# Optimization experiments

Measured on AMD Instinct MI355X. Metric: run time of the kernel, lower is better.

## Reference

```python
import jax, jax.numpy as jnp
import numpy as np

BUCKET_SIZE = 64  # must divide seq_len


def setup_inputs() -> dict:
    key = jax.random.key(0)
    k1, k2, k3, k4 = jax.random.split(key, 4)
    B, S, D = 4, 4096, 1024
    query = jax.random.normal(k1, (B, S, D), dtype=jnp.float32)
    key_t = jax.random.normal(k2, (B, S, D), dtype=jnp.float32)
    value = jax.random.normal(k3, (B, S, D), dtype=jnp.float32)
    # random hashing hyperplanes: [B, D, bucket_size // 2]
    R = jax.random.normal(k4, (B, D, BUCKET_SIZE // 2), dtype=jnp.float32)
    return {"query": query, "key": key_t, "value": value, "R": R}


def reference(query, key, value, R):
    B, S, D = query.shape
    # random projection: [B, S, bucket_size // 2]
    xR = jnp.einsum("bsd,bdr->bsr", query, R)
    # mirror trick -> [B, S, bucket_size]
    concat_xR = jnp.concatenate([xR, -xR], axis=-1)
    buckets = jnp.argmax(concat_xR, axis=-1)          # [B, S] int
    sticker = jnp.argsort(buckets, axis=-1)            # token permutation into buckets
    undo_sort = jnp.argsort(sticker, axis=-1)          # computed in original (unused)
    # batched gather (tf.gather batch_dims=1, axis=1)
    sorted_query = jnp.take_along_axis(query, sticker[..., None], axis=1)
    sorted_value = jnp.take_along_axis(value, sticker[..., None], axis=1)
    # tf.split(x, bucket_size, 1) then stack(axis=1) == reshape to chunks
    chunked_query = sorted_query.reshape(B, BUCKET_SIZE, S // BUCKET_SIZE, D)
    chunked_value = sorted_value.reshape(B, BUCKET_SIZE, S // BUCKET_SIZE, D)
    del undo_sort, chunked_query, chunked_value  # dead code in original; module returns sticker
    return sticker
```

## Files before the change

kernel.cpp:

```cpp
#include <hip/hip_runtime.h>


#define B_DIM 4
#define S_LEN 4096
#define D_DIM 1024
#define NRR 32
#define NBK 64
#define TMK 64
#define NCHUNK (S_LEN / TMK)
#define QB 4096

typedef const __attribute__((address_space(1))) void* gas_t;
typedef __attribute__((address_space(3))) void* las_t;

#define FMA4(A, S, B)                                                        \
    (A).x = fmaf((S), (B).x, (A).x); (A).y = fmaf((S), (B).y, (A).y);        \
    (A).z = fmaf((S), (B).z, (A).z); (A).w = fmaf((S), (B).w, (A).w);

__global__ void __launch_bounds__(256) __attribute__((amdgpu_waves_per_eu(1, 1)))
k1_buckets(const float* __restrict__ Q, const float* __restrict__ R,
           int* __restrict__ buckets, int* __restrict__ hist)
{
    __shared__ float4 smem4[QB + 2048];
    __shared__ int cnt[NBK];

    const int t = threadIdx.x;
    const int b = blockIdx.x >> 6;
    const int chunk = blockIdx.x & 63;

    const int w = t >> 6;
    const int lane = t & 63;
    const int tok_t = lane >> 5;
    const int r_t = (lane >> 3) & 3;
    const int kl = lane & 7;

    const float4* Qw4 = (const float4*)(Q + ((size_t)b * S_LEN + chunk * TMK + w * 16) * D_DIM);
    const float4* Rg4 = (const float4*)(R + (size_t)b * D_DIM * NRR);

#define STAGE_R(H)                                                            \
    {                                                                         \
        _Pragma("unroll")                                                     \
        for (int i = 0; i < 16; ++i) {                                        \
            const int rel = w * 1024 + i * 64 + lane;                         \
            const int kh = rel >> 3, v = rel & 7;                             \
            __builtin_amdgcn_global_load_lds(                                 \
                (gas_t)(Rg4 + ((size_t)(H) * 512 + kh) * 8 + (v ^ ((kh >> 3) & 7))), \
                (las_t)&smem4[w * 1024 + i * 64], 16, 0, 0);                  \
        }                                                                     \
    }

#define ISSUE_Q(H, TILE, DST)                                                 \
    {                                                                         \
        _Pragma("unroll")                                                     \
        for (int i = 0; i < 4; ++i) {                                         \
            const int f = i * 64 + lane;                                      \
            const int td = f >> 4, sd = f & 15;                               \
            __builtin_amdgcn_global_load_lds(                                 \
                (gas_t)(Qw4 + (size_t)td * 256 + (H) * 128 + (TILE) * 16      \
                        + (sd ^ (td >> 3))),                                  \
                (las_t)&smem4[QB + w * 512 + (DST) * 256 + i * 64], 16, 0, 0);\
        }                                                                     \
    }

#define COMPUTE(TILE, BUF)                                                    \
    {                                                                         \
        const float4* qb = smem4 + QB + w * 512 + (BUF) * 256;                \
        const float4* rb = smem4;                                             \
        _Pragma("unroll")                                                     \
        for (int kap = 0; kap < 2; ++kap) {                                   \
            float4 qv[8];                                                     \
            _Pragma("unroll")                                                 \
            for (int j = 0; j < 8; ++j)                                       \
                qv[j] = qb[(tok_t * 8 + j) * 16 + (((kl << 1) + kap) ^ tok_t)];\
            _Pragma("unroll")                                                 \
            for (int c = 0; c < 4; ++c) {                                     \
                const int krow = (TILE) * 64 + kl * 8 + kap * 4 + c;          \
                const float4 rv0 = rb[krow * 8 + ((r_t * 2 + 0) ^ kl)];       \
                const float4 rv1 = rb[krow * 8 + ((r_t * 2 + 1) ^ kl)];       \
                _Pragma("unroll")                                             \
                for (int j = 0; j < 8; ++j) {                                 \
                    const float s = c == 0 ? qv[j].x : c == 1 ? qv[j].y       \
                                  : c == 2 ? qv[j].z : qv[j].w;               \
                    FMA4(acc[j][0], s, rv0);                                  \
                    FMA4(acc[j][1], s, rv1);                                  \
                }                                                             \
            }                                                                 \
        }                                                                     \
    }

    float4 acc[8][2];
#pragma unroll
    for (int j = 0; j < 8; ++j) {
        acc[j][0] = make_float4(0.f, 0.f, 0.f, 0.f);
        acc[j][1] = make_float4(0.f, 0.f, 0.f, 0.f);
    }
    if (t < NBK) cnt[t] = 0;

    for (int h = 0; h < 2; ++h) {
        STAGE_R(h)
        ISSUE_Q(h, 0, 0)
        asm volatile("s_waitcnt vmcnt(0)" ::: "memory");
        __syncthreads();

        for (int tau = 0; tau < 8; ++tau) {
            if (tau < 7) {
                ISSUE_Q(h, tau + 1, (tau + 1) & 1)
                asm volatile("s_waitcnt vmcnt(4)" ::: "memory");
            } else {
                asm volatile("s_waitcnt vmcnt(0)" ::: "memory");
            }
            COMPUTE(tau, tau & 1)
        }
        __syncthreads();
    }
#undef STAGE_R
#undef ISSUE_Q
#undef COMPUTE

#pragma unroll
    for (int j = 0; j < 8; ++j)
#pragma unroll
        for (int p = 0; p < 2; ++p)
#pragma unroll
            for (int off = 1; off < 8; off <<= 1) {
                acc[j][p].x += __shfl_xor(acc[j][p].x, off, 64);
                acc[j][p].y += __shfl_xor(acc[j][p].y, off, 64);
                acc[j][p].z += __shfl_xor(acc[j][p].z, off, 64);
                acc[j][p].w += __shfl_xor(acc[j][p].w, off, 64);
            }

    int bkarr[8];
#pragma unroll
    for (int j = 0; j < 8; ++j) {
        const int rbase = r_t * 8;
        float m1 = acc[j][0].x; int i1 = rbase;
        float m2 = m1;          int i2 = rbase;
#pragma unroll
        for (int p = 0; p < 2; ++p)
#pragma unroll
            for (int c = 0; c < 4; ++c) {
                if (p == 0 && c == 0) continue;
                const float v = p == 0
                    ? (c == 1 ? acc[j][0].y : c == 2 ? acc[j][0].z : acc[j][0].w)
                    : (c == 0 ? acc[j][1].x : c == 1 ? acc[j][1].y
                              : c == 2 ? acc[j][1].z : acc[j][1].w);
                const int r = rbase + p * 4 + c;
                if (v > m1) { m1 = v; i1 = r; }
                if (v < m2) { m2 = v; i2 = r; }
            }
#pragma unroll
        for (int off = 8; off <= 16; off <<= 1) {
            const float om1 = __shfl_xor(m1, off, 64);
            const int   oi1 = __shfl_xor(i1, off, 64);
            const float om2 = __shfl_xor(m2, off, 64);
            const int   oi2 = __shfl_xor(i2, off, 64);
            if (om1 > m1 || (om1 == m1 && oi1 < i1)) { m1 = om1; i1 = oi1; }
            if (om2 < m2 || (om2 == m2 && oi2 < i2)) { m2 = om2; i2 = oi2; }
        }
        bkarr[j] = (m1 >= -m2) ? i1 : (NRR + i2);
    }

    if ((lane & 31) == 0) {
#pragma unroll
        for (int j = 0; j < 8; ++j) {
            const int gtok = chunk * TMK + w * 16 + tok_t * 8 + j;
            buckets[(size_t)b * S_LEN + gtok] = bkarr[j];
            atomicAdd(&cnt[bkarr[j]], 1);
        }
    }
    __syncthreads();
    if (t < NBK) hist[((size_t)b * NCHUNK + chunk) * NBK + t] = cnt[t];
}

__global__ __launch_bounds__(256) void k2_scan(
    const int* __restrict__ hist, int* __restrict__ chunkOffset)
{
    const int t = threadIdx.x;
    const int b = t >> 6;
    const int bk = t & 63;
    const int lane = t & 63;

    int total = 0;
    for (int c = 0; c < NCHUNK; ++c)
        total += hist[((size_t)b * NCHUNK + c) * NBK + bk];

    int incl = total;
#pragma unroll
    for (int off = 1; off < 64; off <<= 1) {
        int n = __shfl_up(incl, off, 64);
        if (lane >= off) incl += n;
    }
    int run = incl - total;

    for (int c = 0; c < NCHUNK; ++c) {
        int h = hist[((size_t)b * NCHUNK + c) * NBK + bk];
        chunkOffset[((size_t)b * NCHUNK + c) * NBK + bk] = run;
        run += h;
    }
}

__global__ __launch_bounds__(256) void k3_scatter(
    const int* __restrict__ buckets, const int* __restrict__ chunkOffset,
    int* __restrict__ out)
{
    const int gid = blockIdx.x * 256 + threadIdx.x;
    const int b = gid >> 12;
    const int s = gid & (S_LEN - 1);
    const int chunk = s >> 6;
    const int lane = threadIdx.x & 63;

    const int bk = buckets[gid];

    unsigned long long m = ~0ull;
#pragma unroll
    for (int i = 0; i < 6; ++i) {
        unsigned long long bi = __ballot((bk >> i) & 1);
        m &= ((bk >> i) & 1) ? bi : ~bi;
    }
    int rank = __popcll(m & ((1ull << lane) - 1ull));

    int pos = chunkOffset[((size_t)b * NCHUNK + chunk) * NBK + bk] + rank;
    out[(size_t)b * S_LEN + pos] = s;
}

extern "C" void kernel_launch(void* const* d_in, const int* in_sizes, int n_in,
                              void* d_out, int out_size, void* d_ws, size_t ws_size,
                              hipStream_t stream) {
    const float* Q = (const float*)d_in[0];
    const float* R = (const float*)d_in[3];

    int* buckets     = (int*)d_ws;
    int* hist        = buckets + B_DIM * S_LEN;
    int* chunkOffset = hist + B_DIM * NCHUNK * NBK;

    k1_buckets<<<B_DIM * NCHUNK, 256, 0, stream>>>(Q, R, buckets, hist);
    k2_scan   <<<1,              256, 0, stream>>>(hist, chunkOffset);
    k3_scatter<<<(B_DIM * S_LEN) / 256, 256, 0, stream>>>(buckets, chunkOffset, (int*)d_out);
}
```

Measured before the change: 39.98 us.

## Split projection GEMM along D into four partial blocks with separate combine kernel

The fused bucket kernel is split so that each (batch, chunk) projection runs as four blocks, each covering a quarter of the D dimension. The blocks write partial dot products to a workspace, and a new combine kernel sums the partials, takes the argmax over the mirrored values and builds the per-chunk histogram. This raises the grid from 256 to 1024 blocks and halves the LDS per block, so more CUs are busy and occupancy goes to two waves per EU. The cost is an extra kernel launch and a round trip of the partial sums through global memory. The in-loop pipelining is also changed: a full vmcnt wait now follows each compute step.

After: 41.03 us. 1.03x slower.

```diff
diff --git a/kernel.cpp b/kernel.cpp
--- a/kernel.cpp
+++ b/kernel.cpp
@@ -8,7 +8,9 @@
 #define NBK 64
 #define TMK 64
 #define NCHUNK (S_LEN / TMK)
-#define QB 4096
+#define NKQ 4
+#define QOFF 2048
+#define PSL 2048
 
 typedef const __attribute__((address_space(1))) void* gas_t;
 typedef __attribute__((address_space(3))) void* las_t;
@@ -17,17 +19,18 @@
     (A).x = fmaf((S), (B).x, (A).x); (A).y = fmaf((S), (B).y, (A).y);        \
     (A).z = fmaf((S), (B).z, (A).z); (A).w = fmaf((S), (B).w, (A).w);
 
-__global__ void __launch_bounds__(256) __attribute__((amdgpu_waves_per_eu(1, 1)))
-k1_buckets(const float* __restrict__ Q, const float* __restrict__ R,
-           int* __restrict__ buckets, int* __restrict__ hist)
-{
-    __shared__ float4 smem4[QB + 2048];
-    __shared__ int cnt[NBK];
+__global__ void __launch_bounds__(256) __attribute__((amdgpu_waves_per_eu(2, 2)))
+k1_gemm(const float* __restrict__ Q, const float* __restrict__ R,
+        float4* __restrict__ P4)
+{
+    __shared__ float4 smem4[QOFF + 2048];
+
+    const int bid = blockIdx.x;
+    const int kqr = bid & 3;
+    const int chunk = (bid >> 2) & 63;
+    const int b = bid >> 8;
 
     const int t = threadIdx.x;
-    const int b = blockIdx.x >> 6;
-    const int chunk = blockIdx.x & 63;
-
     const int w = t >> 6;
     const int lane = t & 63;
     const int tok_t = lane >> 5;
@@ -37,34 +40,34 @@
     const float4* Qw4 = (const float4*)(Q + ((size_t)b * S_LEN + chunk * TMK + w * 16) * D_DIM);
     const float4* Rg4 = (const float4*)(R + (size_t)b * D_DIM * NRR);
 
-#define STAGE_R(H)                                                            \
+#define STAGE_R()                                                             \
     {                                                                         \
         _Pragma("unroll")                                                     \
-        for (int i = 0; i < 16; ++i) {                                        \
-            const int rel = w * 1024 + i * 64 + lane;                         \
+        for (int i = 0; i < 8; ++i) {                                         \
+            const int rel = w * 512 + i * 64 + lane;                          \
             const int kh = rel >> 3, v = rel & 7;                             \
             __builtin_amdgcn_global_load_lds(                                 \
-                (gas_t)(Rg4 + ((size_t)(H) * 512 + kh) * 8 + (v ^ ((kh >> 3) & 7))), \
-                (las_t)&smem4[w * 1024 + i * 64], 16, 0, 0);                  \
+                (gas_t)(Rg4 + ((size_t)kqr * 256 + kh) * 8 + (v ^ ((kh >> 3) & 7))), \
+                (las_t)&smem4[w * 512 + i * 64], 16, 0, 0);                   \
         }                                                                     \
     }
 
-#define ISSUE_Q(H, TILE, DST)                                                 \
+#define ISSUE_Q(TILE, DST)                                                    \
     {                                                                         \
         _Pragma("unroll")                                                     \
         for (int i = 0; i < 4; ++i) {                                         \
             const int f = i * 64 + lane;                                      \
             const int td = f >> 4, sd = f & 15;                               \
             __builtin_amdgcn_global_load_lds(                                 \
-                (gas_t)(Qw4 + (size_t)td * 256 + (H) * 128 + (TILE) * 16      \
+                (gas_t)(Qw4 + (size_t)td * 256 + kqr * 64 + (TILE) * 16       \
                         + (sd ^ (td >> 3))),                                  \
-                (las_t)&smem4[QB + w * 512 + (DST) * 256 + i * 64], 16, 0, 0);\
+                (las_t)&smem4[QOFF + w * 512 + (DST) * 256 + i * 64], 16, 0, 0);\
         }                                                                     \
     }
 
 #define COMPUTE(TILE, BUF)                                                    \
     {                                                                         \
-        const float4* qb = smem4 + QB + w * 512 + (BUF) * 256;                \
+        const float4* qb = smem4 + QOFF + w * 512 + (BUF) * 256;              \
         const float4* rb = smem4;                                             \
         _Pragma("unroll")                                                     \
         for (int kap = 0; kap < 2; ++kap) {                                   \
@@ -94,24 +97,20 @@
         acc[j][0] = make_float4(0.f, 0.f, 0.f, 0.f);
         acc[j][1] = make_float4(0.f, 0.f, 0.f, 0.f);
     }
-    if (t < NBK) cnt[t] = 0;
-
-    for (int h = 0; h < 2; ++h) {
-        STAGE_R(h)
-        ISSUE_Q(h, 0, 0)
+
+    STAGE_R()
+    ISSUE_Q(0, 0)
+    asm volatile("s_waitcnt vmcnt(0)" ::: "memory");
+    __syncthreads();
+
+#pragma unroll
+    for (int tau = 0; tau < 4; ++tau) {
+        if (tau + 1 < 4) {
+            asm volatile("s_waitcnt lgkmcnt(0)" ::: "memory");
+            ISSUE_Q(tau + 1, (tau + 1) & 1)
+        }
+        COMPUTE(tau, tau & 1)
         asm volatile("s_waitcnt vmcnt(0)" ::: "memory");
-        __syncthreads();
-
-        for (int tau = 0; tau < 8; ++tau) {
-            if (tau < 7) {
-                ISSUE_Q(h, tau + 1, (tau + 1) & 1)
-                asm volatile("s_waitcnt vmcnt(4)" ::: "memory");
-            } else {
-                asm volatile("s_waitcnt vmcnt(0)" ::: "memory");
-            }
-            COMPUTE(tau, tau & 1)
-        }
-        __syncthreads();
     }
 #undef STAGE_R
 #undef ISSUE_Q
@@ -129,47 +128,55 @@
                 acc[j][p].w += __shfl_xor(acc[j][p].w, off, 64);
             }
 
-    int bkarr[8];
-#pragma unroll
-    for (int j = 0; j < 8; ++j) {
-        const int rbase = r_t * 8;
-        float m1 = acc[j][0].x; int i1 = rbase;
-        float m2 = m1;          int i2 = rbase;
-#pragma unroll
-        for (int p = 0; p < 2; ++p)
-#pragma unroll
-            for (int c = 0; c < 4; ++c) {
-                if (p == 0 && c == 0) continue;
-                const float v = p == 0
-                    ? (c == 1 ? acc[j][0].y : c == 2 ? acc[j][0].z : acc[j][0].w)
-                    : (c == 0 ? acc[j][1].x : c == 1 ? acc[j][1].y
-                              : c == 2 ? acc[j][1].z : acc[j][1].w);
-                const int r = rbase + p * 4 + c;
-                if (v > m1) { m1 = v; i1 = r; }
-                if (v < m2) { m2 = v; i2 = r; }
-            }
-#pragma unroll
-        for (int off = 8; off <= 16; off <<= 1) {
-            const float om1 = __shfl_xor(m1, off, 64);
-            const int   oi1 = __shfl_xor(i1, off, 64);
-            const float om2 = __shfl_xor(m2, off, 64);
-            const int   oi2 = __shfl_xor(i2, off, 64);
-            if (om1 > m1 || (om1 == m1 && oi1 < i1)) { m1 = om1; i1 = oi1; }
-            if (om2 < m2 || (om2 == m2 && oi2 < i2)) { m2 = om2; i2 = oi2; }
+    if (kl == 0) {
+        float4* Pb = P4 + (((size_t)b * NCHUNK + chunk) * NKQ + kqr) * (PSL / 4);
+#pragma unroll
+        for (int j = 0; j < 8; ++j) {
+            const int tok = w * 16 + tok_t * 8 + j;
+            Pb[tok * 8 + r_t * 2 + 0] = acc[j][0];
+            Pb[tok * 8 + r_t * 2 + 1] = acc[j][1];
         }
-        bkarr[j] = (m1 >= -m2) ? i1 : (NRR + i2);
-    }
-
-    if ((lane & 31) == 0) {
-#pragma unroll
-        for (int j = 0; j < 8; ++j) {
-            const int gtok = chunk * TMK + w * 16 + tok_t * 8 + j;
-            buckets[(size_t)b * S_LEN + gtok] = bkarr[j];
-            atomicAdd(&cnt[bkarr[j]], 1);
+    }
+}
+
+__global__ __launch_bounds__(256) void k1c_combine(
+    const float* __restrict__ P,
+    int* __restrict__ buckets, int* __restrict__ hist)
+{
+    __shared__ float xs[TMK][NRR + 1];
+    __shared__ int cnt[NBK];
+
+    const int bid = blockIdx.x;
+    const int b = bid >> 6;
+    const int h = bid & 63;
+    const int t = threadIdx.x;
+
+    const float* Pb = P + ((size_t)b * NCHUNK + h) * NKQ * PSL;
+#pragma unroll
+    for (int i = 0; i < 8; ++i) {
+        const int idx = t + 256 * i;
+        const int tok = idx >> 5, r = idx & 31;
+        const size_t base = (size_t)tok * NRR + r;
+        xs[tok][r] = Pb[base] + Pb[base + PSL] + Pb[base + 2 * PSL] + Pb[base + 3 * PSL];
+    }
+    if (t < NBK) cnt[t] = 0;
+    __syncthreads();
+
+    if (t < TMK) {
+        float m1 = xs[t][0]; int i1 = 0;
+        float m2 = m1;       int i2 = 0;
+#pragma unroll
+        for (int r = 1; r < NRR; ++r) {
+            const float v = xs[t][r];
+            if (v > m1) { m1 = v; i1 = r; }
+            if (v < m2) { m2 = v; i2 = r; }
         }
+        const int bk = (m1 >= -m2) ? i1 : (NRR + i2);
+        buckets[(size_t)b * S_LEN + h * TMK + t] = bk;
+        atomicAdd(&cnt[bk], 1);
     }
     __syncthreads();
-    if (t < NBK) hist[((size_t)b * NCHUNK + chunk) * NBK + t] = cnt[t];
+    if (t < NBK) hist[((size_t)b * NCHUNK + h) * NBK + t] = cnt[t];
 }
 
 __global__ __launch_bounds__(256) void k2_scan(
@@ -229,11 +236,13 @@
     const float* Q = (const float*)d_in[0];
     const float* R = (const float*)d_in[3];
 
-    int* buckets     = (int*)d_ws;
+    float* P         = (float*)d_ws;
+    int* buckets     = (int*)(P + (size_t)B_DIM * NCHUNK * NKQ * PSL);
     int* hist        = buckets + B_DIM * S_LEN;
     int* chunkOffset = hist + B_DIM * NCHUNK * NBK;
 
-    k1_buckets<<<B_DIM * NCHUNK, 256, 0, stream>>>(Q, R, buckets, hist);
-    k2_scan   <<<1,              256, 0, stream>>>(hist, chunkOffset);
-    k3_scatter<<<(B_DIM * S_LEN) / 256, 256, 0, stream>>>(buckets, chunkOffset, (int*)d_out);
-}
+    k1_gemm    <<<B_DIM * NCHUNK * NKQ, 256, 0, stream>>>(Q, R, (float4*)P);
+    k1c_combine<<<B_DIM * NCHUNK,       256, 0, stream>>>(P, buckets, hist);
+    k2_scan    <<<1,                    256, 0, stream>>>(hist, chunkOffset);
+    k3_scatter <<<(B_DIM * S_LEN) / 256, 256, 0, stream>>>(buckets, chunkOffset, (int*)d_out);
+}
```
